# Kernel optimization log

Measured on AMD Instinct MI355X. Metric: run time of the kernel, lower is better.

## Reference

```python
import math
import jax, jax.numpy as jnp
import numpy as np

B, S, D, H = 128, 512, 768, 12
DH = D // H  # 64


def setup_inputs() -> dict:
    key = jax.random.key(0)
    k1, k2, k3, k4, k5 = jax.random.split(key, 5)
    return {
        "X": jax.random.normal(k1, (B, S, D), jnp.float32),
        "W_qkv": jax.random.normal(k2, (3 * D, D), jnp.float32) * 0.02,
        "b_qkv": jax.random.normal(k3, (3 * D,), jnp.float32) * 0.02,
        "W_dense": jax.random.normal(k4, (D, D), jnp.float32) * 0.02,
        "b_dense": jax.random.normal(k5, (D,), jnp.float32) * 0.02,
    }


def reference(X, W_qkv, b_qkv, W_dense, b_dense):
    # Faithful translation of SelfAttention.forward (including its unusual
    # seq/batch layout: scores are [S*H, B, B] and the tril mask FILLS the
    # lower triangle with -10000, exactly as masked_fill_(tril, -1e4) does).
    b, s, d = X.shape
    qkv = jnp.einsum('bsd,ed->bse', X, W_qkv) + b_qkv            # [B,S,3D]
    qkv = qkv.reshape(b, s, H, 3 * DH)
    q = qkv[..., :DH]
    k = qkv[..., DH:2 * DH]
    v = qkv[..., 2 * DH:]
    q = q.reshape(b, s * H, DH).transpose(1, 0, 2)               # [S*H,B,DH]
    k = k.reshape(b, s * H, DH).transpose(1, 0, 2)
    v = v.reshape(b, s * H, DH).transpose(1, 0, 2)
    scores = jnp.einsum('nbd,ncd->nbc', q, k) / math.sqrt(DH)    # [S*H,B,B]
    scores = scores.reshape(s, H, b, b)
    tril = jnp.tril(jnp.ones((s, b, b), bool))[:, None]          # [S,1,B,B]
    scores = jnp.where(tril, jnp.float32(-10000.0), scores)
    probs = jax.nn.softmax(scores, axis=-1).reshape(s * H, b, b)
    ctx = jnp.einsum('nbc,ncd->nbd', probs, v)                   # [S*H,B,DH]
    ctx = ctx.reshape(s, H, b, DH).transpose(2, 0, 1, 3).reshape(b, s, d)
    out = jnp.einsum('bsd,ed->bse', ctx, W_dense)                # bias NOT added
    return (out, b_dense)
```

## Files before the change

kernel.cpp:

```cpp
#include <hip/hip_runtime.h>
#include <hip/hip_bf16.h>
#include <cstdint>
#include <cstddef>


typedef __attribute__((ext_vector_type(8))) short bf16x8_t;
typedef __attribute__((ext_vector_type(4))) float f32x4_t;

__device__ inline unsigned short f2bf(float x) {
  union { float f; unsigned int u; } v; v.f = x;
  return (unsigned short)((v.u + 0x7FFFu + ((v.u >> 16) & 1u)) >> 16);
}

#define GLL16(gp, lp) __builtin_amdgcn_global_load_lds(                      \
    (const __attribute__((address_space(1))) void*)(gp),                     \
    (__attribute__((address_space(3))) void*)(lp), 16, 0, 0)

__global__ __launch_bounds__(256) void cvt_kernel(const float* __restrict__ in,
                                                  unsigned short* __restrict__ out,
                                                  int n4) {
  int i = blockIdx.x * 256 + threadIdx.x;
  if (i >= n4) return;
  const float4 v = ((const float4*)in)[i];
  ushort4 o;
  o.x = f2bf(v.x); o.y = f2bf(v.y); o.z = f2bf(v.z); o.w = f2bf(v.w);
  ((ushort4*)out)[i] = o;
}

__global__ void bias_tail(const float* __restrict__ b, float* __restrict__ out) {
  int i = blockIdx.x * 256 + threadIdx.x;
  if (i < 768) out[(size_t)128 * 512 * 768 + i] = b[i];
}

__global__ __launch_bounds__(256) void gemm_qkv(
    const unsigned short* __restrict__ A,
    const unsigned short* __restrict__ Bt,
    const float* __restrict__ bias,
    unsigned short* __restrict__ QKV) {
  __shared__ unsigned short As[128 * 64];
  __shared__ unsigned short Bs[128 * 64];
  const int tid = threadIdx.x;
  const int wave = tid >> 6, lane = tid & 63;
  const int lane15 = lane & 15, quad = lane >> 4;
  const int mBase = blockIdx.x * 128;
  const int nBase = blockIdx.y * 128;
  const int wm = (wave >> 1) * 64;
  const int wn = (wave & 1) * 64;

  f32x4_t acc[4][4];
#pragma unroll
  for (int i = 0; i < 4; ++i)
#pragma unroll
    for (int j = 0; j < 4; ++j) { f32x4_t z = {0.f, 0.f, 0.f, 0.f}; acc[i][j] = z; }

  const int r16 = lane & 15;
  const int ck8 = (lane >> 4) * 8;
  const unsigned short* Ag = A + (size_t)(mBase + wave * 32 + r16) * 768 + ck8;
  const unsigned short* Bg = Bt + (size_t)(nBase + wave * 32 + r16) * 768 + ck8;
  unsigned short* lA = &As[wave * 4 * 512];
  unsigned short* lB = &Bs[wave * 4 * 512];

  const int aSub = (wm >> 4) * 2;
  const int bSub = (wn >> 4) * 2;

  for (int k0 = 0; k0 < 768; k0 += 64) {
    GLL16(Ag + k0, lA);
    GLL16(Ag + k0 + 32, lA + 512);
    GLL16(Ag + 16 * 768 + k0, lA + 1024);
    GLL16(Ag + 16 * 768 + k0 + 32, lA + 1536);
    GLL16(Bg + k0, lB);
    GLL16(Bg + k0 + 32, lB + 512);
    GLL16(Bg + 16 * 768 + k0, lB + 1024);
    GLL16(Bg + 16 * 768 + k0 + 32, lB + 1536);
    __syncthreads();
#pragma unroll
    for (int kh = 0; kh < 2; ++kh) {
      bf16x8_t aF[4], bF[4];
#pragma unroll
      for (int im = 0; im < 4; ++im)
        aF[im] = *(const bf16x8_t*)&As[(aSub + im * 2 + kh) * 512 + lane * 8];
#pragma unroll
      for (int in = 0; in < 4; ++in)
        bF[in] = *(const bf16x8_t*)&Bs[(bSub + in * 2 + kh) * 512 + lane * 8];
#pragma unroll
      for (int im = 0; im < 4; ++im)
#pragma unroll
        for (int in = 0; in < 4; ++in)
          acc[im][in] = __builtin_amdgcn_mfma_f32_16x16x32_bf16(aF[im], bF[in], acc[im][in], 0, 0, 0);
    }
    __syncthreads();
  }

  float bv[4];
#pragma unroll
  for (int in = 0; in < 4; ++in) bv[in] = bias[nBase + wn + in * 16 + lane15];

#pragma unroll
  for (int im = 0; im < 4; ++im) {
#pragma unroll
    for (int r = 0; r < 4; ++r) {
      const int m = mBase + wm + im * 16 + quad * 4 + r;
      unsigned short* orow = QKV + (size_t)m * 2304 + nBase + wn + lane15;
#pragma unroll
      for (int in = 0; in < 4; ++in)
        orow[in * 16] = f2bf(acc[im][in][r] + bv[in]);
    }
  }
}

__global__ __launch_bounds__(256) void attn_kernel(
    const unsigned short* __restrict__ QKV,
    unsigned short* __restrict__ Ctx) {
  __shared__ unsigned short Qs[128 * 72];
  __shared__ unsigned short Ks[128 * 72];

  const int n = blockIdx.x;
  const int s = n / 12;
  const int h = n - s * 12;
  const int tid = threadIdx.x;
  const int wave = tid >> 6, lane = tid & 63;
  const int lane15 = lane & 15, quad = lane >> 4;

#pragma unroll
  for (int it = 0; it < 4; ++it) {
    const int idx = it * 256 + tid;
    const int bb = idx >> 3, seg = idx & 7;
    const size_t g = (size_t)(bb * 512 + s) * 2304 + h * 192 + seg * 8;
    *(uint4*)&Qs[bb * 72 + seg * 8] = *(const uint4*)&QKV[g];
    *(uint4*)&Ks[bb * 72 + seg * 8] = *(const uint4*)&QKV[g + 64];
  }
  __syncthreads();

  f32x4_t sc[2][8];
#pragma unroll
  for (int im = 0; im < 2; ++im)
#pragma unroll
    for (int in = 0; in < 8; ++in) { f32x4_t z = {0.f, 0.f, 0.f, 0.f}; sc[im][in] = z; }

#pragma unroll
  for (int kk = 0; kk < 2; ++kk) {
    bf16x8_t a0 = *(const bf16x8_t*)&Qs[(wave * 32 + lane15) * 72 + kk * 32 + quad * 8];
    bf16x8_t a1 = *(const bf16x8_t*)&Qs[(wave * 32 + 16 + lane15) * 72 + kk * 32 + quad * 8];
#pragma unroll
    for (int in = 0; in < 8; ++in) {
      bf16x8_t b = *(const bf16x8_t*)&Ks[(in * 16 + lane15) * 72 + kk * 32 + quad * 8];
      sc[0][in] = __builtin_amdgcn_mfma_f32_16x16x32_bf16(a0, b, sc[0][in], 0, 0, 0);
      sc[1][in] = __builtin_amdgcn_mfma_f32_16x16x32_bf16(a1, b, sc[1][in], 0, 0, 0);
    }
  }
  __syncthreads();

  unsigned short* Vt = Ks;
  unsigned short* Ps = Qs;
  {
    const int c = tid & 127, half = tid >> 7;
    const size_t vb = (size_t)(c * 512 + s) * 2304 + h * 192 + 128;
#pragma unroll
    for (int dd = 0; dd < 4; ++dd) {
      const int dseg = half * 4 + dd;
      uint4 v = *(const uint4*)&QKV[vb + dseg * 8];
      const unsigned short* pv = (const unsigned short*)&v;
#pragma unroll
      for (int j = 0; j < 8; ++j) Vt[(dseg * 8 + j) * 136 + c] = pv[j];
    }
  }

  unsigned short* myP = Ps + wave * 16 * 136;

#pragma unroll 1
  for (int im = 0; im < 2; ++im) {
#pragma unroll
    for (int r = 0; r < 4; ++r) {
      const int row = wave * 32 + im * 16 + quad * 4 + r;
      float vals[8];
      float mx = -3.0e38f;
#pragma unroll
      for (int in = 0; in < 8; ++in) {
        const int col = in * 16 + lane15;
        float v = sc[im][in][r] * 0.125f;
        v = (col <= row) ? -10000.0f : v;
        vals[in] = v;
        mx = fmaxf(mx, v);
      }
      mx = fmaxf(mx, __shfl_xor(mx, 1, 16));
      mx = fmaxf(mx, __shfl_xor(mx, 2, 16));
      mx = fmaxf(mx, __shfl_xor(mx, 4, 16));
      mx = fmaxf(mx, __shfl_xor(mx, 8, 16));
      float sum = 0.f;
#pragma unroll
      for (int in = 0; in < 8; ++in) {
        const float e_ = __expf(vals[in] - mx);
        vals[in] = e_;
        sum += e_;
      }
      sum += __shfl_xor(sum, 1, 16);
      sum += __shfl_xor(sum, 2, 16);
      sum += __shfl_xor(sum, 4, 16);
      sum += __shfl_xor(sum, 8, 16);
      const float inv = 1.0f / sum;
#pragma unroll
      for (int in = 0; in < 8; ++in)
        myP[(quad * 4 + r) * 136 + in * 16 + lane15] = f2bf(vals[in] * inv);
    }
    __syncthreads();

    f32x4_t oc[4];
#pragma unroll
    for (int nt = 0; nt < 4; ++nt) { f32x4_t z = {0.f, 0.f, 0.f, 0.f}; oc[nt] = z; }
#pragma unroll
    for (int kk = 0; kk < 4; ++kk) {
      bf16x8_t a = *(const bf16x8_t*)&myP[lane15 * 136 + kk * 32 + quad * 8];
#pragma unroll
      for (int nt = 0; nt < 4; ++nt) {
        bf16x8_t b = *(const bf16x8_t*)&Vt[(nt * 16 + lane15) * 136 + kk * 32 + quad * 8];
        oc[nt] = __builtin_amdgcn_mfma_f32_16x16x32_bf16(a, b, oc[nt], 0, 0, 0);
      }
    }
#pragma unroll
    for (int nt = 0; nt < 4; ++nt) {
#pragma unroll
      for (int r = 0; r < 4; ++r) {
        const int bb = wave * 32 + im * 16 + quad * 4 + r;
        Ctx[((size_t)bb * 512 + s) * 768 + h * 64 + nt * 16 + lane15] = f2bf(oc[nt][r]);
      }
    }
    __syncthreads();
  }
}

__global__ __launch_bounds__(256) void gemm_out(
    const unsigned short* __restrict__ A,
    const unsigned short* __restrict__ Bt,
    float* __restrict__ Out) {
  __shared__ unsigned short As[128 * 64];
  __shared__ unsigned short Bs[128 * 64];
  const int tid = threadIdx.x;
  const int wave = tid >> 6, lane = tid & 63;
  const int lane15 = lane & 15, quad = lane >> 4;
  const int mBase = blockIdx.x * 128;
  const int nBase = blockIdx.y * 128;
  const int wm = (wave >> 1) * 64;
  const int wn = (wave & 1) * 64;

  f32x4_t acc[4][4];
#pragma unroll
  for (int i = 0; i < 4; ++i)
#pragma unroll
    for (int j = 0; j < 4; ++j) { f32x4_t z = {0.f, 0.f, 0.f, 0.f}; acc[i][j] = z; }

  const int r16 = lane & 15;
  const int ck8 = (lane >> 4) * 8;
  const unsigned short* Ag = A + (size_t)(mBase + wave * 32 + r16) * 768 + ck8;
  const unsigned short* Bg = Bt + (size_t)(nBase + wave * 32 + r16) * 768 + ck8;
  unsigned short* lA = &As[wave * 4 * 512];
  unsigned short* lB = &Bs[wave * 4 * 512];

  const int aSub = (wm >> 4) * 2;
  const int bSub = (wn >> 4) * 2;

  for (int k0 = 0; k0 < 768; k0 += 64) {
    GLL16(Ag + k0, lA);
    GLL16(Ag + k0 + 32, lA + 512);
    GLL16(Ag + 16 * 768 + k0, lA + 1024);
    GLL16(Ag + 16 * 768 + k0 + 32, lA + 1536);
    GLL16(Bg + k0, lB);
    GLL16(Bg + k0 + 32, lB + 512);
    GLL16(Bg + 16 * 768 + k0, lB + 1024);
    GLL16(Bg + 16 * 768 + k0 + 32, lB + 1536);
    __syncthreads();
#pragma unroll
    for (int kh = 0; kh < 2; ++kh) {
      bf16x8_t aF[4], bF[4];
#pragma unroll
      for (int im = 0; im < 4; ++im)
        aF[im] = *(const bf16x8_t*)&As[(aSub + im * 2 + kh) * 512 + lane * 8];
#pragma unroll
      for (int in = 0; in < 4; ++in)
        bF[in] = *(const bf16x8_t*)&Bs[(bSub + in * 2 + kh) * 512 + lane * 8];
#pragma unroll
      for (int im = 0; im < 4; ++im)
#pragma unroll
        for (int in = 0; in < 4; ++in)
          acc[im][in] = __builtin_amdgcn_mfma_f32_16x16x32_bf16(aF[im], bF[in], acc[im][in], 0, 0, 0);
    }
    __syncthreads();
  }

#pragma unroll
  for (int im = 0; im < 4; ++im) {
#pragma unroll
    for (int r = 0; r < 4; ++r) {
      const int m = mBase + wm + im * 16 + quad * 4 + r;
      float* orow = Out + (size_t)m * 768 + nBase + wn + lane15;
#pragma unroll
      for (int in = 0; in < 4; ++in)
        orow[in * 16] = acc[im][in][r];
    }
  }
}

extern "C" void kernel_launch(void* const* d_in, const int* in_sizes, int n_in,
                              void* d_out, int out_size, void* d_ws, size_t ws_size,
                              hipStream_t stream) {
  const float* X    = (const float*)d_in[0];
  const float* Wqkv = (const float*)d_in[1];
  const float* bqkv = (const float*)d_in[2];
  const float* Wd   = (const float*)d_in[3];
  const float* bd   = (const float*)d_in[4];
  float* out = (float*)d_out;

  char* ws = (char*)d_ws;
  unsigned short* Xb  = (unsigned short*)(ws);
  unsigned short* QKV = (unsigned short*)(ws + 100663296);
  unsigned short* Wqb = (unsigned short*)(ws + 402653184);
  unsigned short* Wdb = (unsigned short*)(ws + 406192128);

  cvt_kernel<<<dim3(49152), 256, 0, stream>>>(X, Xb, 12582912);
  cvt_kernel<<<dim3(1728), 256, 0, stream>>>(Wqkv, Wqb, 442368);
  cvt_kernel<<<dim3(576), 256, 0, stream>>>(Wd, Wdb, 147456);
  bias_tail<<<dim3(3), 256, 0, stream>>>(bd, out);

  gemm_qkv<<<dim3(512, 18), 256, 0, stream>>>(Xb, Wqb, bqkv, QKV);
  attn_kernel<<<dim3(6144), 256, 0, stream>>>(QKV, Xb );
  gemm_out<<<dim3(512, 6), 256, 0, stream>>>(Xb, Wdb, out);
}
```

Baseline: 1.263 ms.

## Replace both GEMMs with a 256x256-tile double-buffered pipelined 8-wave kernel

Both projection GEMMs now go through one templated kernel that uses 256x256 tiles, 512 threads and double-buffered LDS. The next K-tile is loaded with global_load_lds and interleaved with the MFMA phases, using explicit vmcnt waits, raw barriers and s_setprio around the MFMA blocks. The goal is to hide global-load latency behind compute and raise arithmetic intensity per block. In exchange, the 128 KB of LDS and large accumulator arrays limit occupancy, and the out-projection gets only 768 blocks.

```diff
diff --git a/kernel.cpp b/kernel.cpp
--- a/kernel.cpp
+++ b/kernel.cpp
@@ -15,6 +15,13 @@
 #define GLL16(gp, lp) __builtin_amdgcn_global_load_lds(                      \
     (const __attribute__((address_space(1))) void*)(gp),                     \
     (__attribute__((address_space(3))) void*)(lp), 16, 0, 0)
+
+__device__ __forceinline__ void bar() {
+  asm volatile("" ::: "memory");
+  __builtin_amdgcn_s_barrier();
+  asm volatile("" ::: "memory");
+}
+#define WAITV(n) asm volatile("s_waitcnt vmcnt(" #n ")" ::: "memory")
 
 __global__ __launch_bounds__(256) void cvt_kernel(const float* __restrict__ in,
                                                   unsigned short* __restrict__ out,
@@ -32,78 +39,148 @@
   if (i < 768) out[(size_t)128 * 512 * 768 + i] = b[i];
 }
 
-__global__ __launch_bounds__(256) void gemm_qkv(
+template <bool BF16OUT>
+__global__ __launch_bounds__(512, 2) void gemm256(
     const unsigned short* __restrict__ A,
     const unsigned short* __restrict__ Bt,
     const float* __restrict__ bias,
-    unsigned short* __restrict__ QKV) {
-  __shared__ unsigned short As[128 * 64];
-  __shared__ unsigned short Bs[128 * 64];
+    unsigned short* __restrict__ outB,
+    float* __restrict__ outF,
+    const int ldo) {
+  __shared__ unsigned short As[2 * 16384];
+  __shared__ unsigned short Bs[2 * 16384];
+
   const int tid = threadIdx.x;
   const int wave = tid >> 6, lane = tid & 63;
   const int lane15 = lane & 15, quad = lane >> 4;
-  const int mBase = blockIdx.x * 128;
-  const int nBase = blockIdx.y * 128;
-  const int wm = (wave >> 1) * 64;
-  const int wn = (wave & 1) * 64;
-
-  f32x4_t acc[4][4];
-#pragma unroll
-  for (int i = 0; i < 4; ++i)
+  const int wm = wave >> 2, wn = wave & 3;
+  const int mBase = blockIdx.y * 256;
+  const int nBase = blockIdx.x * 256;
+
+  f32x4_t acc[8][4];
+#pragma unroll
+  for (int i = 0; i < 8; ++i)
 #pragma unroll
     for (int j = 0; j < 4; ++j) { f32x4_t z = {0.f, 0.f, 0.f, 0.f}; acc[i][j] = z; }
 
-  const int r16 = lane & 15;
-  const int ck8 = (lane >> 4) * 8;
-  const unsigned short* Ag = A + (size_t)(mBase + wave * 32 + r16) * 768 + ck8;
-  const unsigned short* Bg = Bt + (size_t)(nBase + wave * 32 + r16) * 768 + ck8;
-  unsigned short* lA = &As[wave * 4 * 512];
-  unsigned short* lB = &Bs[wave * 4 * 512];
-
-  const int aSub = (wm >> 4) * 2;
-  const int bSub = (wn >> 4) * 2;
-
-  for (int k0 = 0; k0 < 768; k0 += 64) {
-    GLL16(Ag + k0, lA);
-    GLL16(Ag + k0 + 32, lA + 512);
-    GLL16(Ag + 16 * 768 + k0, lA + 1024);
-    GLL16(Ag + 16 * 768 + k0 + 32, lA + 1536);
-    GLL16(Bg + k0, lB);
-    GLL16(Bg + k0 + 32, lB + 512);
-    GLL16(Bg + 16 * 768 + k0, lB + 1024);
-    GLL16(Bg + 16 * 768 + k0 + 32, lB + 1536);
-    __syncthreads();
-#pragma unroll
-    for (int kh = 0; kh < 2; ++kh) {
-      bf16x8_t aF[4], bF[4];
-#pragma unroll
-      for (int im = 0; im < 4; ++im)
-        aF[im] = *(const bf16x8_t*)&As[(aSub + im * 2 + kh) * 512 + lane * 8];
+  const unsigned short* Ag = A + (size_t)(mBase + wave * 32 + lane15) * 768 + quad * 8;
+  const unsigned short* Bg = Bt + (size_t)(nBase + wave * 32 + lane15) * 768 + quad * 8;
+
+#define STAGE_A(t_, ro_) do {                                                 \
+    const unsigned short* s_ = Ag + (size_t)(ro_) * (16 * 768) + (t_) * 64;   \
+    unsigned short* d_ = &As[(((t_) & 1) << 14) + (2 * wave + (ro_)) * 1024]; \
+    GLL16(s_, d_); GLL16(s_ + 32, d_ + 512);                                  \
+  } while (0)
+#define STAGE_B(t_, ro_) do {                                                 \
+    const unsigned short* s_ = Bg + (size_t)(ro_) * (16 * 768) + (t_) * 64;   \
+    unsigned short* d_ = &Bs[(((t_) & 1) << 14) + (2 * wave + (ro_)) * 1024]; \
+    GLL16(s_, d_); GLL16(s_ + 32, d_ + 512);                                  \
+  } while (0)
+
+  const unsigned short* aB = &As[(wm * 8) * 1024 + lane * 8];
+  const unsigned short* bB = &Bs[(wn * 4) * 1024 + lane * 8];
+#define RA(buf_, im_, kk_) (*(const bf16x8_t*)&aB[(buf_) + ((im_) * 2 + (kk_)) * 512])
+#define RB(buf_, in_, kk_) (*(const bf16x8_t*)&bB[(buf_) + ((in_) * 2 + (kk_)) * 512])
+
+  STAGE_A(0, 0); STAGE_A(0, 1); STAGE_B(0, 0); STAGE_B(0, 1);
+  STAGE_A(1, 0);
+  WAITV(2);
+  bar();
+
+  const int NT = 12;
+#pragma unroll 1
+  for (int t = 0; t < NT; ++t) {
+    const int buf = (t & 1) << 14;
+    bf16x8_t a0[4], b0[4];
+#pragma unroll
+    for (int im = 0; im < 4; ++im) a0[im] = RA(buf, im, 0);
+#pragma unroll
+    for (int in = 0; in < 4; ++in) b0[in] = RB(buf, in, 0);
+    if (t + 1 < NT) STAGE_A(t + 1, 1);
+    bar();
+    __builtin_amdgcn_s_setprio(1);
+#pragma unroll
+    for (int im = 0; im < 4; ++im)
 #pragma unroll
       for (int in = 0; in < 4; ++in)
-        bF[in] = *(const bf16x8_t*)&Bs[(bSub + in * 2 + kh) * 512 + lane * 8];
-#pragma unroll
-      for (int im = 0; im < 4; ++im)
+        acc[im][in] = __builtin_amdgcn_mfma_f32_16x16x32_bf16(a0[im], b0[in], acc[im][in], 0, 0, 0);
+    __builtin_amdgcn_s_setprio(0);
+    bar();
+    bf16x8_t a1[4], a0k[4], b1[4];
+#pragma unroll
+    for (int im = 0; im < 4; ++im) a1[im] = RA(buf, im + 4, 0);
+#pragma unroll
+    for (int im = 0; im < 4; ++im) a0k[im] = RA(buf, im, 1);
+#pragma unroll
+    for (int in = 0; in < 4; ++in) b1[in] = RB(buf, in, 1);
+    if (t + 1 < NT) STAGE_B(t + 1, 0);
+    bar();
+    __builtin_amdgcn_s_setprio(1);
+#pragma unroll
+    for (int im = 0; im < 4; ++im)
+#pragma unroll
+      for (int in = 0; in < 4; ++in)
+        acc[im + 4][in] = __builtin_amdgcn_mfma_f32_16x16x32_bf16(a1[im], b0[in], acc[im + 4][in], 0, 0, 0);
+    __builtin_amdgcn_s_setprio(0);
+    bar();
+    bf16x8_t a1k[4];
+#pragma unroll
+    for (int im = 0; im < 4; ++im) a1k[im] = RA(buf, im + 4, 1);
+    if (t + 1 < NT) STAGE_B(t + 1, 1);
+    bar();
+    __builtin_amdgcn_s_setprio(1);
+#pragma unroll
+    for (int im = 0; im < 4; ++im)
+#pragma unroll
+      for (int in = 0; in < 4; ++in)
+        acc[im][in] = __builtin_amdgcn_mfma_f32_16x16x32_bf16(a0k[im], b1[in], acc[im][in], 0, 0, 0);
+    __builtin_amdgcn_s_setprio(0);
+    bar();
+    if (t + 2 < NT) STAGE_A(t + 2, 0);
+    bar();
+    __builtin_amdgcn_s_setprio(1);
+#pragma unroll
+    for (int im = 0; im < 4; ++im)
+#pragma unroll
+      for (int in = 0; in < 4; ++in)
+        acc[im + 4][in] = __builtin_amdgcn_mfma_f32_16x16x32_bf16(a1k[im], b1[in], acc[im + 4][in], 0, 0, 0);
+    __builtin_amdgcn_s_setprio(0);
+    if (t < NT - 1) {
+      if (t + 2 < NT) { WAITV(2); } else { WAITV(0); }
+      bar();
+    }
+  }
+#undef STAGE_A
+#undef STAGE_B
+#undef RA
+#undef RB
+
+  if constexpr (BF16OUT) {
+    float bv[4];
+#pragma unroll
+    for (int in = 0; in < 4; ++in) bv[in] = bias[nBase + wn * 64 + in * 16 + lane15];
+#pragma unroll
+    for (int im = 0; im < 8; ++im) {
+#pragma unroll
+      for (int r = 0; r < 4; ++r) {
+        const int m = mBase + wm * 128 + im * 16 + quad * 4 + r;
+        unsigned short* orow = outB + (size_t)m * ldo + nBase + wn * 64 + lane15;
 #pragma unroll
         for (int in = 0; in < 4; ++in)
-          acc[im][in] = __builtin_amdgcn_mfma_f32_16x16x32_bf16(aF[im], bF[in], acc[im][in], 0, 0, 0);
-    }
-    __syncthreads();
-  }
-
-  float bv[4];
-#pragma unroll
-  for (int in = 0; in < 4; ++in) bv[in] = bias[nBase + wn + in * 16 + lane15];
-
-#pragma unroll
-  for (int im = 0; im < 4; ++im) {
-#pragma unroll
-    for (int r = 0; r < 4; ++r) {
-      const int m = mBase + wm + im * 16 + quad * 4 + r;
-      unsigned short* orow = QKV + (size_t)m * 2304 + nBase + wn + lane15;
-#pragma unroll
-      for (int in = 0; in < 4; ++in)
-        orow[in * 16] = f2bf(acc[im][in][r] + bv[in]);
+          orow[in * 16] = f2bf(acc[im][in][r] + bv[in]);
+      }
+    }
+  } else {
+#pragma unroll
+    for (int im = 0; im < 8; ++im) {
+#pragma unroll
+      for (int r = 0; r < 4; ++r) {
+        const int m = mBase + wm * 128 + im * 16 + quad * 4 + r;
+        float* orow = outF + (size_t)m * ldo + nBase + wn * 64 + lane15;
+#pragma unroll
+        for (int in = 0; in < 4; ++in)
+          orow[in * 16] = acc[im][in][r];
+      }
     }
   }
 }
@@ -225,77 +302,6 @@
       }
     }
     __syncthreads();
-  }
-}
-
-__global__ __launch_bounds__(256) void gemm_out(
-    const unsigned short* __restrict__ A,
-    const unsigned short* __restrict__ Bt,
-    float* __restrict__ Out) {
-  __shared__ unsigned short As[128 * 64];
-  __shared__ unsigned short Bs[128 * 64];
-  const int tid = threadIdx.x;
-  const int wave = tid >> 6, lane = tid & 63;
-  const int lane15 = lane & 15, quad = lane >> 4;
-  const int mBase = blockIdx.x * 128;
-  const int nBase = blockIdx.y * 128;
-  const int wm = (wave >> 1) * 64;
-  const int wn = (wave & 1) * 64;
-
-  f32x4_t acc[4][4];
-#pragma unroll
-  for (int i = 0; i < 4; ++i)
-#pragma unroll
-    for (int j = 0; j < 4; ++j) { f32x4_t z = {0.f, 0.f, 0.f, 0.f}; acc[i][j] = z; }
-
-  const int r16 = lane & 15;
-  const int ck8 = (lane >> 4) * 8;
-  const unsigned short* Ag = A + (size_t)(mBase + wave * 32 + r16) * 768 + ck8;
-  const unsigned short* Bg = Bt + (size_t)(nBase + wave * 32 + r16) * 768 + ck8;
-  unsigned short* lA = &As[wave * 4 * 512];
-  unsigned short* lB = &Bs[wave * 4 * 512];
-
-  const int aSub = (wm >> 4) * 2;
-  const int bSub = (wn >> 4) * 2;
-
-  for (int k0 = 0; k0 < 768; k0 += 64) {
-    GLL16(Ag + k0, lA);
-    GLL16(Ag + k0 + 32, lA + 512);
-    GLL16(Ag + 16 * 768 + k0, lA + 1024);
-    GLL16(Ag + 16 * 768 + k0 + 32, lA + 1536);
-    GLL16(Bg + k0, lB);
-    GLL16(Bg + k0 + 32, lB + 512);
-    GLL16(Bg + 16 * 768 + k0, lB + 1024);
-    GLL16(Bg + 16 * 768 + k0 + 32, lB + 1536);
-    __syncthreads();
-#pragma unroll
-    for (int kh = 0; kh < 2; ++kh) {
-      bf16x8_t aF[4], bF[4];
-#pragma unroll
-      for (int im = 0; im < 4; ++im)
-        aF[im] = *(const bf16x8_t*)&As[(aSub + im * 2 + kh) * 512 + lane * 8];
-#pragma unroll
-      for (int in = 0; in < 4; ++in)
-        bF[in] = *(const bf16x8_t*)&Bs[(bSub + in * 2 + kh) * 512 + lane * 8];
-#pragma unroll
-      for (int im = 0; im < 4; ++im)
-#pragma unroll
-        for (int in = 0; in < 4; ++in)
-          acc[im][in] = __builtin_amdgcn_mfma_f32_16x16x32_bf16(aF[im], bF[in], acc[im][in], 0, 0, 0);
-    }
-    __syncthreads();
-  }
-
-#pragma unroll
-  for (int im = 0; im < 4; ++im) {
-#pragma unroll
-    for (int r = 0; r < 4; ++r) {
-      const int m = mBase + wm + im * 16 + quad * 4 + r;
-      float* orow = Out + (size_t)m * 768 + nBase + wn + lane15;
-#pragma unroll
-      for (int in = 0; in < 4; ++in)
-        orow[in * 16] = acc[im][in][r];
-    }
   }
 }
 
@@ -320,7 +326,7 @@
   cvt_kernel<<<dim3(576), 256, 0, stream>>>(Wd, Wdb, 147456);
   bias_tail<<<dim3(3), 256, 0, stream>>>(bd, out);
 
-  gemm_qkv<<<dim3(512, 18), 256, 0, stream>>>(Xb, Wqb, bqkv, QKV);
+  gemm256<true><<<dim3(9, 256), 512, 0, stream>>>(Xb, Wqb, bqkv, QKV, nullptr, 2304);
   attn_kernel<<<dim3(6144), 256, 0, stream>>>(QKV, Xb );
-  gemm_out<<<dim3(512, 6), 256, 0, stream>>>(Xb, Wdb, out);
-}
+  gemm256<false><<<dim3(3, 256), 512, 0, stream>>>(Xb, Wdb, nullptr, nullptr, out, 768);
+}
```

Measured after the change: 1.101 ms. -12.8%, faster.
